# Optimization experiments

Hardware: AMD Instinct MI355X
Metric: run time of the kernel (lower is better)

The kernel has to match this reference:

```python
import jax, jax.numpy as jnp
import numpy as np

D_HEAD = 64
SCALE = D_HEAD ** 0.5
MASK_FILL = -10000.0


def setup_inputs() -> dict:
    key = jax.random.key(0)
    kq, kk, kv, km = jax.random.split(key, 4)
    B, H, S, D = 2, 16, 2048, D_HEAD
    query = jax.random.normal(kq, (B, H, S, D), dtype=jnp.float32)
    k = jax.random.normal(kk, (B, H, S, D), dtype=jnp.float32)
    v = jax.random.normal(kv, (B, H, S, D), dtype=jnp.float32)
    attn_mask = jax.random.randint(km, (B, H, S, S), 0, 2).astype(jnp.bool_)
    return {"query": query, "key": k, "value": v, "attn_mask": attn_mask}


def reference(query, key, value, attn_mask):
    # scores: [B, H, Sq, Sk]
    scores = jnp.einsum("bhqd,bhkd->bhqk", query, key) / SCALE
    scores = jnp.where(attn_mask, MASK_FILL, scores)
    attn_prob = jax.nn.softmax(scores, axis=-1)
    context = jnp.einsum("bhqk,bhkd->bhqd", attn_prob, value)
    return (context, attn_prob)
```

## Files before the change

kernel.cpp:

```cpp
#include <hip/hip_runtime.h>
#include <cstdint>
#include <cstddef>

#define S_LEN 2048
#define D_HEAD 64
#define NBH 32

typedef __attribute__((ext_vector_type(8))) short short8;
typedef __attribute__((ext_vector_type(8))) unsigned short ushort8;
typedef __attribute__((ext_vector_type(4))) unsigned short us4;
typedef __attribute__((ext_vector_type(4))) unsigned int ui4;
typedef __attribute__((ext_vector_type(4))) float floatx4;

__device__ __forceinline__ unsigned short f2bf(float f){
  union { float f; unsigned int i; } v; v.f = f;
  unsigned int u = v.i;
  u += 0x7fffu + ((u >> 16) & 1u);
  return (unsigned short)(u >> 16);
}
__device__ __forceinline__ float bf2f(unsigned short u){
  union { unsigned int i; float f; } v; v.i = ((unsigned int)u) << 16; return v.f;
}

__device__ __forceinline__ int swz(int row, int col){
  return row * S_LEN + ((((col >> 3) ^ row) & 15) << 3)
                     + (((col >> 3) & ~15) << 3) + (col & 7);
}

__global__ void detect_mask_kernel(const unsigned int* __restrict__ m, int* __restrict__ flag){
  __shared__ int f;
  if (threadIdx.x == 0) f = 0;
  __syncthreads();
  if (m[threadIdx.x] > 1u) atomicOr(&f, 1);
  __syncthreads();
  if (threadIdx.x == 0) *flag = f;
}

__global__ void convK_kernel(const float* __restrict__ K, unsigned short* __restrict__ Kb){
  const size_t i = ((size_t)blockIdx.x * 256 + threadIdx.x) * 8;
  floatx4 x0 = *(const floatx4*)(K + i);
  floatx4 x1 = *(const floatx4*)(K + i + 4);
  ushort8 o;
#pragma unroll
  for (int j = 0; j < 4; ++j){ o[j] = f2bf(x0[j]); o[4 + j] = f2bf(x1[j]); }
  *(ushort8*)(Kb + i) = o;
}

__global__ void vtrans_kernel(const float* __restrict__ V, unsigned short* __restrict__ Vt){
  const int bh = blockIdx.y;
  const int n  = threadIdx.x & 63;
  const int k0 = blockIdx.x * 32 + (threadIdx.x >> 6) * 8;
  const float* Vp = V + (size_t)bh * S_LEN * D_HEAD;
  ushort8 o;
#pragma unroll
  for (int i = 0; i < 8; ++i) o[i] = f2bf(Vp[(size_t)(k0 + i) * D_HEAD + n]);
  *(ushort8*)(Vt + (size_t)bh * D_HEAD * S_LEN + (size_t)n * S_LEN + k0) = o;
}

__global__ __launch_bounds__(256, 2) void attn_kernel(
    const float* __restrict__ Q, const unsigned short* __restrict__ Kb,
    const void* __restrict__ maskp, const int* __restrict__ flag,
    const unsigned short* __restrict__ Vt,
    float* __restrict__ prob, float* __restrict__ ctx,
    float* __restrict__ redg, float* __restrict__ invg){

  __shared__ unsigned short Pt[16 * S_LEN];

  const int lin  = blockIdx.y * gridDim.x + blockIdx.x;
  const int xcd  = lin & 7;
  const int sub  = lin >> 3;
  const int bh   = xcd * 4 + (sub & 3);
  const int qt   = sub >> 2;

  const int q0g  = bh * S_LEN + qt * 16;
  const int tid  = threadIdx.x;
  const int wave = tid >> 6;
  const int lane = tid & 63;
  const int quad = lane >> 4;
  const int r16  = lane & 15;
  const int blk  = bh * gridDim.x + qt;

  const float* qrow = Q + (size_t)(q0g + r16) * D_HEAD + quad * 8;
  short8 a0, a1;
  {
    floatx4 x0 = *(const floatx4*)(qrow);
    floatx4 x1 = *(const floatx4*)(qrow + 4);
    floatx4 y0 = *(const floatx4*)(qrow + 32);
    floatx4 y1 = *(const floatx4*)(qrow + 36);
#pragma unroll
    for (int j = 0; j < 4; ++j){
      a0[j] = (short)f2bf(x0[j]); a0[4 + j] = (short)f2bf(x1[j]);
      a1[j] = (short)f2bf(y0[j]); a1[4 + j] = (short)f2bf(y1[j]);
    }
  }

  const bool mInt = (*flag) == 0;
  const unsigned int*  mI = (const unsigned int*)maskp;
  const unsigned char* mB = (const unsigned char*)maskp;
  const size_t mrow = (size_t)(q0g + r16) * S_LEN;

  float racc = 0.f;

#pragma unroll 2
  for (int t = 0; t < 32; ++t){
    const int s0 = wave * 512 + t * 16;
    const unsigned short* krow = Kb + (size_t)(bh * S_LEN + s0 + r16) * D_HEAD + quad * 8;
    const short8 b0 = *(const short8*)(krow);
    const short8 b1 = *(const short8*)(krow + 32);
    unsigned int mm[4];
    if (mInt){
      const ui4 m4 = *(const ui4*)(mI + mrow + s0 + quad * 4);
#pragma unroll
      for (int i = 0; i < 4; ++i) mm[i] = m4[i];
    } else {
      const unsigned int mv = *(const unsigned int*)(mB + mrow + s0 + quad * 4);
#pragma unroll
      for (int i = 0; i < 4; ++i) mm[i] = (mv >> (8 * i)) & 0xffu;
    }
    floatx4 c = {0.f, 0.f, 0.f, 0.f};
    c = __builtin_amdgcn_mfma_f32_16x16x32_bf16(b0, a0, c, 0, 0, 0);
    c = __builtin_amdgcn_mfma_f32_16x16x32_bf16(b1, a1, c, 0, 0, 0);
    us4 w;
#pragma unroll
    for (int i = 0; i < 4; ++i){
      const float p = mm[i] ? 0.0f : __expf(c[i] * 0.125f);
      racc += p;
      w[i] = f2bf(p);
    }
    *(us4*)(&Pt[swz(r16, s0 + quad * 4)]) = w;
  }

  racc += __shfl_xor(racc, 16);
  racc += __shfl_xor(racc, 32);
  if (lane < 16) redg[(size_t)blk * 64 + wave * 16 + lane] = racc;
  __syncthreads();
  if (tid < 16){
    float s = 0.f;
#pragma unroll
    for (int w = 0; w < 4; ++w) s += redg[(size_t)blk * 64 + w * 16 + tid];
    invg[(size_t)blk * 16 + tid] = (s > 0.f) ? (1.0f / s) : 0.0f;
  }
  __syncthreads();

  float inv4[4];
#pragma unroll
  for (int i = 0; i < 4; ++i) inv4[i] = invg[(size_t)blk * 16 + quad * 4 + i];

  const unsigned short* vrow = Vt + (size_t)bh * D_HEAD * S_LEN
                                  + (size_t)(wave * 16 + r16) * S_LEN + quad * 8;
  floatx4 c = {0.f, 0.f, 0.f, 0.f};
#pragma unroll 4
  for (int kk = 0; kk < 64; ++kk){
    const short8 b = *(const short8*)(vrow + kk * 32);
    const short8 a = *(const short8*)(&Pt[swz(r16, kk * 32 + quad * 8)]);
    c = __builtin_amdgcn_mfma_f32_16x16x32_bf16(a, b, c, 0, 0, 0);
  }
#pragma unroll
  for (int i = 0; i < 4; ++i)
    ctx[(size_t)(q0g + quad * 4 + i) * D_HEAD + wave * 16 + r16] = c[i] * inv4[i];

#pragma unroll
  for (int rr = 0; rr < 4; ++rr){
    const int row = wave * 4 + rr;
    const float iv = invg[(size_t)blk * 16 + row];
    float* pg = prob + (size_t)(q0g + row) * S_LEN;
#pragma unroll
    for (int j = 0; j < 4; ++j){
      const int col = j * 512 + lane * 8;
      const ushort8 u = *(const ushort8*)(&Pt[swz(row, col)]);
      floatx4 o0, o1;
#pragma unroll
      for (int e = 0; e < 4; ++e){
        o0[e] = bf2f(u[e]) * iv;
        o1[e] = bf2f(u[4 + e]) * iv;
      }
      *(floatx4*)(pg + col)     = o0;
      *(floatx4*)(pg + col + 4) = o1;
    }
  }
}

extern "C" void kernel_launch(void* const* d_in, const int* in_sizes, int n_in,
                              void* d_out, int out_size, void* d_ws, size_t ws_size,
                              hipStream_t stream) {
  const float* Q = (const float*)d_in[0];
  const float* K = (const float*)d_in[1];
  const float* V = (const float*)d_in[2];
  const void*  M = d_in[3];

  float* ctx  = (float*)d_out;
  float* prob = (float*)d_out + (size_t)NBH * S_LEN * D_HEAD;

  int*   flag = (int*)d_ws;
  float* redg = (float*)((char*)d_ws + (1u << 12));
  float* invg = (float*)((char*)d_ws + (1u << 12) + (1u << 20));
  unsigned short* Kb = (unsigned short*)((char*)d_ws + (2u << 20));
  unsigned short* Vt = (unsigned short*)((char*)d_ws + (10u << 20));

  hipLaunchKernelGGL(detect_mask_kernel, dim3(1), dim3(256), 0, stream,
                     (const unsigned int*)M, flag);
  hipLaunchKernelGGL(convK_kernel, dim3(2048), dim3(256), 0, stream, K, Kb);
  hipLaunchKernelGGL(vtrans_kernel, dim3(S_LEN/32, NBH), dim3(256), 0, stream, V, Vt);
  hipLaunchKernelGGL(attn_kernel, dim3(S_LEN/16, NBH), dim3(256), 0, stream,
                     Q, Kb, M, flag, Vt, prob, ctx, redg, invg);
}
```

Before: 1.103 ms.

## Recompute scores in second pass, drop LDS staging, permute P in registers

Each wave now owns 16 query rows across the full key length. A first pass computes only the row sums, and a second pass recomputes QK^T and exp, writes normalized probabilities straight to global memory, and feeds P into the PV MFMA via ds_bpermute register shuffles. This removes the 64KB LDS buffer, the cross-wave reduction through global memory, and the block syncs, which allows higher occupancy (launch bounds 4). The cost is doubled QK MFMA, exp and mask-read work, with the mask now read twice from memory.

```diff
diff --git a/kernel.cpp b/kernel.cpp
--- a/kernel.cpp
+++ b/kernel.cpp
@@ -8,7 +8,6 @@
 
 typedef __attribute__((ext_vector_type(8))) short short8;
 typedef __attribute__((ext_vector_type(8))) unsigned short ushort8;
-typedef __attribute__((ext_vector_type(4))) unsigned short us4;
 typedef __attribute__((ext_vector_type(4))) unsigned int ui4;
 typedef __attribute__((ext_vector_type(4))) float floatx4;
 
@@ -18,13 +17,8 @@
   u += 0x7fffu + ((u >> 16) & 1u);
   return (unsigned short)(u >> 16);
 }
-__device__ __forceinline__ float bf2f(unsigned short u){
-  union { unsigned int i; float f; } v; v.i = ((unsigned int)u) << 16; return v.f;
-}
-
-__device__ __forceinline__ int swz(int row, int col){
-  return row * S_LEN + ((((col >> 3) ^ row) & 15) << 3)
-                     + (((col >> 3) & ~15) << 3) + (col & 7);
+__device__ __forceinline__ unsigned int pk2bf(float lo, float hi){
+  return ((unsigned int)f2bf(hi) << 16) | (unsigned int)f2bf(lo);
 }
 
 __global__ void detect_mask_kernel(const unsigned int* __restrict__ m, int* __restrict__ flag){
@@ -57,28 +51,24 @@
   *(ushort8*)(Vt + (size_t)bh * D_HEAD * S_LEN + (size_t)n * S_LEN + k0) = o;
 }
 
-__global__ __launch_bounds__(256, 2) void attn_kernel(
+__global__ __launch_bounds__(256, 4) void attn_kernel(
     const float* __restrict__ Q, const unsigned short* __restrict__ Kb,
     const void* __restrict__ maskp, const int* __restrict__ flag,
     const unsigned short* __restrict__ Vt,
-    float* __restrict__ prob, float* __restrict__ ctx,
-    float* __restrict__ redg, float* __restrict__ invg){
-
-  __shared__ unsigned short Pt[16 * S_LEN];
+    float* __restrict__ prob, float* __restrict__ ctx){
 
   const int lin  = blockIdx.y * gridDim.x + blockIdx.x;
   const int xcd  = lin & 7;
   const int sub  = lin >> 3;
   const int bh   = xcd * 4 + (sub & 3);
-  const int qt   = sub >> 2;
-
-  const int q0g  = bh * S_LEN + qt * 16;
-  const int tid  = threadIdx.x;
-  const int wave = tid >> 6;
-  const int lane = tid & 63;
+  const int qb   = sub >> 2;
+
+  const int wave = threadIdx.x >> 6;
+  const int lane = threadIdx.x & 63;
   const int quad = lane >> 4;
   const int r16  = lane & 15;
-  const int blk  = bh * gridDim.x + qt;
+
+  const int q0g = bh * S_LEN + qb * 64 + wave * 16;
 
   const float* qrow = Q + (size_t)(q0g + r16) * D_HEAD + quad * 8;
   short8 a0, a1;
@@ -95,88 +85,125 @@
   }
 
   const bool mInt = (*flag) == 0;
-  const unsigned int*  mI = (const unsigned int*)maskp;
-  const unsigned char* mB = (const unsigned char*)maskp;
-  const size_t mrow = (size_t)(q0g + r16) * S_LEN;
+  const unsigned int*  mI = (const unsigned int*)maskp + (size_t)(q0g + r16) * S_LEN;
+  const unsigned char* mB = (const unsigned char*)maskp + (size_t)(q0g + r16) * S_LEN;
+  const unsigned short* kbase = Kb + (size_t)bh * S_LEN * D_HEAD;
 
   float racc = 0.f;
-
 #pragma unroll 2
-  for (int t = 0; t < 32; ++t){
-    const int s0 = wave * 512 + t * 16;
-    const unsigned short* krow = Kb + (size_t)(bh * S_LEN + s0 + r16) * D_HEAD + quad * 8;
+  for (int t = 0; t < 128; ++t){
+    const unsigned short* krow = kbase + (size_t)(t * 16 + r16) * D_HEAD + quad * 8;
     const short8 b0 = *(const short8*)(krow);
     const short8 b1 = *(const short8*)(krow + 32);
     unsigned int mm[4];
     if (mInt){
-      const ui4 m4 = *(const ui4*)(mI + mrow + s0 + quad * 4);
+      const ui4 m4 = *(const ui4*)(mI + t * 16 + quad * 4);
 #pragma unroll
       for (int i = 0; i < 4; ++i) mm[i] = m4[i];
     } else {
-      const unsigned int mv = *(const unsigned int*)(mB + mrow + s0 + quad * 4);
+      const unsigned int mv = *(const unsigned int*)(mB + t * 16 + quad * 4);
 #pragma unroll
       for (int i = 0; i < 4; ++i) mm[i] = (mv >> (8 * i)) & 0xffu;
     }
     floatx4 c = {0.f, 0.f, 0.f, 0.f};
     c = __builtin_amdgcn_mfma_f32_16x16x32_bf16(b0, a0, c, 0, 0, 0);
     c = __builtin_amdgcn_mfma_f32_16x16x32_bf16(b1, a1, c, 0, 0, 0);
-    us4 w;
-#pragma unroll
-    for (int i = 0; i < 4; ++i){
-      const float p = mm[i] ? 0.0f : __expf(c[i] * 0.125f);
-      racc += p;
-      w[i] = f2bf(p);
-    }
-    *(us4*)(&Pt[swz(r16, s0 + quad * 4)]) = w;
-  }
-
+#pragma unroll
+    for (int i = 0; i < 4; ++i)
+      racc += mm[i] ? 0.0f : __expf(c[i] * 0.125f);
+  }
   racc += __shfl_xor(racc, 16);
   racc += __shfl_xor(racc, 32);
-  if (lane < 16) redg[(size_t)blk * 64 + wave * 16 + lane] = racc;
-  __syncthreads();
-  if (tid < 16){
-    float s = 0.f;
-#pragma unroll
-    for (int w = 0; w < 4; ++w) s += redg[(size_t)blk * 64 + w * 16 + tid];
-    invg[(size_t)blk * 16 + tid] = (s > 0.f) ? (1.0f / s) : 0.0f;
-  }
-  __syncthreads();
+  const float inv = (racc > 0.f) ? (1.0f / racc) : 0.0f;
+
+  float* prow = prob + (size_t)(q0g + r16) * S_LEN;
+  const unsigned short* vbase = Vt + (size_t)bh * D_HEAD * S_LEN
+                                   + (size_t)r16 * S_LEN + quad * 8;
+  floatx4 cc0 = {0.f,0.f,0.f,0.f}, cc1 = {0.f,0.f,0.f,0.f};
+  floatx4 cc2 = {0.f,0.f,0.f,0.f}, cc3 = {0.f,0.f,0.f,0.f};
+
+  for (int u = 0; u < 64; ++u){
+    const unsigned short* krow = kbase + (size_t)(u * 32 + r16) * D_HEAD + quad * 8;
+    const short8 b00 = *(const short8*)(krow);
+    const short8 b01 = *(const short8*)(krow + 32);
+    const short8 b10 = *(const short8*)(krow + 16 * D_HEAD);
+    const short8 b11 = *(const short8*)(krow + 16 * D_HEAD + 32);
+    unsigned int m0[4], m1[4];
+    if (mInt){
+      const ui4 w0 = *(const ui4*)(mI + u * 32 + quad * 4);
+      const ui4 w1 = *(const ui4*)(mI + u * 32 + 16 + quad * 4);
+#pragma unroll
+      for (int i = 0; i < 4; ++i){ m0[i] = w0[i]; m1[i] = w1[i]; }
+    } else {
+      const unsigned int v0m = *(const unsigned int*)(mB + u * 32 + quad * 4);
+      const unsigned int v1m = *(const unsigned int*)(mB + u * 32 + 16 + quad * 4);
+#pragma unroll
+      for (int i = 0; i < 4; ++i){
+        m0[i] = (v0m >> (8 * i)) & 0xffu;
+        m1[i] = (v1m >> (8 * i)) & 0xffu;
+      }
+    }
+    floatx4 c0 = {0.f,0.f,0.f,0.f}, c1 = {0.f,0.f,0.f,0.f};
+    c0 = __builtin_amdgcn_mfma_f32_16x16x32_bf16(b00, a0, c0, 0, 0, 0);
+    c0 = __builtin_amdgcn_mfma_f32_16x16x32_bf16(b01, a1, c0, 0, 0, 0);
+    c1 = __builtin_amdgcn_mfma_f32_16x16x32_bf16(b10, a0, c1, 0, 0, 0);
+    c1 = __builtin_amdgcn_mfma_f32_16x16x32_bf16(b11, a1, c1, 0, 0, 0);
+
+    float p0[4], p1[4];
+#pragma unroll
+    for (int i = 0; i < 4; ++i){
+      p0[i] = m0[i] ? 0.0f : __expf(c0[i] * 0.125f);
+      p1[i] = m1[i] ? 0.0f : __expf(c1[i] * 0.125f);
+    }
+
+    floatx4 o0, o1;
+#pragma unroll
+    for (int i = 0; i < 4; ++i){ o0[i] = p0[i] * inv; o1[i] = p1[i] * inv; }
+    *(floatx4*)(prow + u * 32 + quad * 4)      = o0;
+    *(floatx4*)(prow + u * 32 + 16 + quad * 4) = o1;
+
+    const int pl0 = (int)pk2bf(p0[0], p0[1]);
+    const int pl1 = (int)pk2bf(p0[2], p0[3]);
+    const int pl2 = (int)pk2bf(p1[0], p1[1]);
+    const int pl3 = (int)pk2bf(p1[2], p1[3]);
+
+    const int idx0 = (r16 + ((quad & 1) << 5)) << 2;
+    const int idx1 = idx0 + 64;
+    const int t0a = __builtin_amdgcn_ds_bpermute(idx0, pl0);
+    const int t0b = __builtin_amdgcn_ds_bpermute(idx0, pl2);
+    const int t1a = __builtin_amdgcn_ds_bpermute(idx0, pl1);
+    const int t1b = __builtin_amdgcn_ds_bpermute(idx0, pl3);
+    const int t2a = __builtin_amdgcn_ds_bpermute(idx1, pl0);
+    const int t2b = __builtin_amdgcn_ds_bpermute(idx1, pl2);
+    const int t3a = __builtin_amdgcn_ds_bpermute(idx1, pl1);
+    const int t3b = __builtin_amdgcn_ds_bpermute(idx1, pl3);
+    const bool hi = quad >= 2;
+    union { int d[4]; short8 s; } af;
+    af.d[0] = hi ? t0b : t0a;
+    af.d[1] = hi ? t1b : t1a;
+    af.d[2] = hi ? t2b : t2a;
+    af.d[3] = hi ? t3b : t3a;
+
+    const short8 v0 = *(const short8*)(vbase + u * 32);
+    const short8 v1 = *(const short8*)(vbase + 16 * S_LEN + u * 32);
+    const short8 v2 = *(const short8*)(vbase + 32 * S_LEN + u * 32);
+    const short8 v3 = *(const short8*)(vbase + 48 * S_LEN + u * 32);
+    cc0 = __builtin_amdgcn_mfma_f32_16x16x32_bf16(af.s, v0, cc0, 0, 0, 0);
+    cc1 = __builtin_amdgcn_mfma_f32_16x16x32_bf16(af.s, v1, cc1, 0, 0, 0);
+    cc2 = __builtin_amdgcn_mfma_f32_16x16x32_bf16(af.s, v2, cc2, 0, 0, 0);
+    cc3 = __builtin_amdgcn_mfma_f32_16x16x32_bf16(af.s, v3, cc3, 0, 0, 0);
+  }
 
   float inv4[4];
 #pragma unroll
-  for (int i = 0; i < 4; ++i) inv4[i] = invg[(size_t)blk * 16 + quad * 4 + i];
-
-  const unsigned short* vrow = Vt + (size_t)bh * D_HEAD * S_LEN
-                                  + (size_t)(wave * 16 + r16) * S_LEN + quad * 8;
-  floatx4 c = {0.f, 0.f, 0.f, 0.f};
-#pragma unroll 4
-  for (int kk = 0; kk < 64; ++kk){
-    const short8 b = *(const short8*)(vrow + kk * 32);
-    const short8 a = *(const short8*)(&Pt[swz(r16, kk * 32 + quad * 8)]);
-    c = __builtin_amdgcn_mfma_f32_16x16x32_bf16(a, b, c, 0, 0, 0);
-  }
-#pragma unroll
-  for (int i = 0; i < 4; ++i)
-    ctx[(size_t)(q0g + quad * 4 + i) * D_HEAD + wave * 16 + r16] = c[i] * inv4[i];
-
-#pragma unroll
-  for (int rr = 0; rr < 4; ++rr){
-    const int row = wave * 4 + rr;
-    const float iv = invg[(size_t)blk * 16 + row];
-    float* pg = prob + (size_t)(q0g + row) * S_LEN;
-#pragma unroll
-    for (int j = 0; j < 4; ++j){
-      const int col = j * 512 + lane * 8;
-      const ushort8 u = *(const ushort8*)(&Pt[swz(row, col)]);
-      floatx4 o0, o1;
-#pragma unroll
-      for (int e = 0; e < 4; ++e){
-        o0[e] = bf2f(u[e]) * iv;
-        o1[e] = bf2f(u[4 + e]) * iv;
-      }
-      *(floatx4*)(pg + col)     = o0;
-      *(floatx4*)(pg + col + 4) = o1;
-    }
+  for (int i = 0; i < 4; ++i) inv4[i] = __shfl(inv, quad * 4 + i, 64);
+#pragma unroll
+  for (int i = 0; i < 4; ++i){
+    float* cr = ctx + (size_t)(q0g + quad * 4 + i) * D_HEAD + r16;
+    cr[ 0] = cc0[i] * inv4[i];
+    cr[16] = cc1[i] * inv4[i];
+    cr[32] = cc2[i] * inv4[i];
+    cr[48] = cc3[i] * inv4[i];
   }
 }
 
@@ -192,8 +219,6 @@
   float* prob = (float*)d_out + (size_t)NBH * S_LEN * D_HEAD;
 
   int*   flag = (int*)d_ws;
-  float* redg = (float*)((char*)d_ws + (1u << 12));
-  float* invg = (float*)((char*)d_ws + (1u << 12) + (1u << 20));
   unsigned short* Kb = (unsigned short*)((char*)d_ws + (2u << 20));
   unsigned short* Vt = (unsigned short*)((char*)d_ws + (10u << 20));
 
@@ -201,6 +226,6 @@
                      (const unsigned int*)M, flag);
   hipLaunchKernelGGL(convK_kernel, dim3(2048), dim3(256), 0, stream, K, Kb);
   hipLaunchKernelGGL(vtrans_kernel, dim3(S_LEN/32, NBH), dim3(256), 0, stream, V, Vt);
-  hipLaunchKernelGGL(attn_kernel, dim3(S_LEN/16, NBH), dim3(256), 0, stream,
-                     Q, Kb, M, flag, Vt, prob, ctx, redg, invg);
-}
+  hipLaunchKernelGGL(attn_kernel, dim3(S_LEN/64, NBH), dim3(256), 0, stream,
+                     Q, Kb, M, flag, Vt, prob, ctx);
+}
```

Result: slower. 1.285 ms (+16.5%).

## Pre-pack attention mask into bitmask and split PV accumulators

Applied to the files above, without the earlier changes.

A new pre-pass kernel compresses the boolean or int mask into one bit per element, writing it into the not-yet-written context region of the output buffer. The attention kernel then loads one prefetched vector of packed bits per eight score tiles instead of a per-tile mask load. This is meant to shorten the latency-bound mask reads in the QK loop. In exchange it adds a separate full pass over the mask plus a 16MB write and re-read. The PV loop also uses two independent MFMA accumulators to break the dependency chain.

```diff
diff --git a/kernel.cpp b/kernel.cpp
--- a/kernel.cpp
+++ b/kernel.cpp
@@ -34,6 +34,36 @@
   if (m[threadIdx.x] > 1u) atomicOr(&f, 1);
   __syncthreads();
   if (threadIdx.x == 0) *flag = f;
+}
+
+__global__ void packmask_kernel(const void* __restrict__ maskp, const int* __restrict__ flag,
+                                unsigned int* __restrict__ pm){
+  const int w = blockIdx.x * 256 + threadIdx.x;
+  unsigned int bits = 0;
+  if (*flag){
+    const unsigned char* mb = (const unsigned char*)maskp + (size_t)w * 32;
+    const ui4 x0 = *(const ui4*)(mb);
+    const ui4 x1 = *(const ui4*)(mb + 16);
+#pragma unroll
+    for (int i = 0; i < 4; ++i){
+      const unsigned int a = x0[i], b = x1[i];
+#pragma unroll
+      for (int j = 0; j < 4; ++j){
+        bits |= (((a >> (8 * j)) & 0xffu) ? 1u : 0u) << (4 * i + j);
+        bits |= (((b >> (8 * j)) & 0xffu) ? 1u : 0u) << (16 + 4 * i + j);
+      }
+    }
+  } else {
+    const unsigned int* mi = (const unsigned int*)maskp + (size_t)w * 32;
+#pragma unroll
+    for (int i = 0; i < 8; ++i){
+      const ui4 x = *(const ui4*)(mi + i * 4);
+#pragma unroll
+      for (int j = 0; j < 4; ++j)
+        bits |= (x[j] ? 1u : 0u) << (i * 4 + j);
+    }
+  }
+  pm[w] = bits;
 }
 
 __global__ void convK_kernel(const float* __restrict__ K, unsigned short* __restrict__ Kb){
@@ -59,7 +89,7 @@
 
 __global__ __launch_bounds__(256, 2) void attn_kernel(
     const float* __restrict__ Q, const unsigned short* __restrict__ Kb,
-    const void* __restrict__ maskp, const int* __restrict__ flag,
+    const unsigned int* __restrict__ pm,
     const unsigned short* __restrict__ Vt,
     float* __restrict__ prob, float* __restrict__ ctx,
     float* __restrict__ redg, float* __restrict__ invg){
@@ -94,40 +124,34 @@
     }
   }
 
-  const bool mInt = (*flag) == 0;
-  const unsigned int*  mI = (const unsigned int*)maskp;
-  const unsigned char* mB = (const unsigned char*)maskp;
-  const size_t mrow = (size_t)(q0g + r16) * S_LEN;
+  const unsigned int* mrow = pm + (size_t)(q0g + r16) * 64 + wave * 16;
+  const unsigned short* kbase = Kb + (size_t)bh * S_LEN * D_HEAD;
 
   float racc = 0.f;
-
-#pragma unroll 2
-  for (int t = 0; t < 32; ++t){
-    const int s0 = wave * 512 + t * 16;
-    const unsigned short* krow = Kb + (size_t)(bh * S_LEN + s0 + r16) * D_HEAD + quad * 8;
-    const short8 b0 = *(const short8*)(krow);
-    const short8 b1 = *(const short8*)(krow + 32);
-    unsigned int mm[4];
-    if (mInt){
-      const ui4 m4 = *(const ui4*)(mI + mrow + s0 + quad * 4);
-#pragma unroll
-      for (int i = 0; i < 4; ++i) mm[i] = m4[i];
-    } else {
-      const unsigned int mv = *(const unsigned int*)(mB + mrow + s0 + quad * 4);
-#pragma unroll
-      for (int i = 0; i < 4; ++i) mm[i] = (mv >> (8 * i)) & 0xffu;
-    }
-    floatx4 c = {0.f, 0.f, 0.f, 0.f};
-    c = __builtin_amdgcn_mfma_f32_16x16x32_bf16(b0, a0, c, 0, 0, 0);
-    c = __builtin_amdgcn_mfma_f32_16x16x32_bf16(b1, a1, c, 0, 0, 0);
-    us4 w;
-#pragma unroll
-    for (int i = 0; i < 4; ++i){
-      const float p = mm[i] ? 0.0f : __expf(c[i] * 0.125f);
-      racc += p;
-      w[i] = f2bf(p);
-    }
-    *(us4*)(&Pt[swz(r16, s0 + quad * 4)]) = w;
+  ui4 mcur = *(const ui4*)(mrow);
+  for (int tt = 0; tt < 4; ++tt){
+    const ui4 mnext = (tt < 3) ? *(const ui4*)(mrow + (tt + 1) * 4) : mcur;
+#pragma unroll
+    for (int tj = 0; tj < 8; ++tj){
+      const int t  = tt * 8 + tj;
+      const int s0 = wave * 512 + t * 16;
+      const unsigned short* krow = kbase + (size_t)(s0 + r16) * D_HEAD + quad * 8;
+      const short8 b0 = *(const short8*)(krow);
+      const short8 b1 = *(const short8*)(krow + 32);
+      floatx4 c = {0.f, 0.f, 0.f, 0.f};
+      c = __builtin_amdgcn_mfma_f32_16x16x32_bf16(b0, a0, c, 0, 0, 0);
+      c = __builtin_amdgcn_mfma_f32_16x16x32_bf16(b1, a1, c, 0, 0, 0);
+      const unsigned int bits = mcur[tj >> 1] >> (16 * (tj & 1) + 4 * quad);
+      us4 w;
+#pragma unroll
+      for (int i = 0; i < 4; ++i){
+        const float p = ((bits >> i) & 1u) ? 0.0f : __expf(c[i] * 0.125f);
+        racc += p;
+        w[i] = f2bf(p);
+      }
+      *(us4*)(&Pt[swz(r16, s0 + quad * 4)]) = w;
+    }
+    mcur = mnext;
   }
 
   racc += __shfl_xor(racc, 16);
@@ -148,16 +172,19 @@
 
   const unsigned short* vrow = Vt + (size_t)bh * D_HEAD * S_LEN
                                   + (size_t)(wave * 16 + r16) * S_LEN + quad * 8;
-  floatx4 c = {0.f, 0.f, 0.f, 0.f};
-#pragma unroll 4
-  for (int kk = 0; kk < 64; ++kk){
-    const short8 b = *(const short8*)(vrow + kk * 32);
-    const short8 a = *(const short8*)(&Pt[swz(r16, kk * 32 + quad * 8)]);
-    c = __builtin_amdgcn_mfma_f32_16x16x32_bf16(a, b, c, 0, 0, 0);
+  floatx4 cA = {0.f,0.f,0.f,0.f}, cB = {0.f,0.f,0.f,0.f};
+#pragma unroll 8
+  for (int kk = 0; kk < 64; kk += 2){
+    const short8 bv0 = *(const short8*)(vrow + kk * 32);
+    const short8 aa0 = *(const short8*)(&Pt[swz(r16, kk * 32 + quad * 8)]);
+    const short8 bv1 = *(const short8*)(vrow + (kk + 1) * 32);
+    const short8 aa1 = *(const short8*)(&Pt[swz(r16, (kk + 1) * 32 + quad * 8)]);
+    cA = __builtin_amdgcn_mfma_f32_16x16x32_bf16(aa0, bv0, cA, 0, 0, 0);
+    cB = __builtin_amdgcn_mfma_f32_16x16x32_bf16(aa1, bv1, cB, 0, 0, 0);
   }
 #pragma unroll
   for (int i = 0; i < 4; ++i)
-    ctx[(size_t)(q0g + quad * 4 + i) * D_HEAD + wave * 16 + r16] = c[i] * inv4[i];
+    ctx[(size_t)(q0g + quad * 4 + i) * D_HEAD + wave * 16 + r16] = (cA[i] + cB[i]) * inv4[i];
 
 #pragma unroll
   for (int rr = 0; rr < 4; ++rr){
@@ -191,6 +218,8 @@
   float* ctx  = (float*)d_out;
   float* prob = (float*)d_out + (size_t)NBH * S_LEN * D_HEAD;
 
+  unsigned int* pm = (unsigned int*)d_out;
+
   int*   flag = (int*)d_ws;
   float* redg = (float*)((char*)d_ws + (1u << 12));
   float* invg = (float*)((char*)d_ws + (1u << 12) + (1u << 20));
@@ -199,8 +228,10 @@
 
   hipLaunchKernelGGL(detect_mask_kernel, dim3(1), dim3(256), 0, stream,
                      (const unsigned int*)M, flag);
+  hipLaunchKernelGGL(packmask_kernel, dim3((NBH * S_LEN * S_LEN / 32) / 256), dim3(256),
+                     0, stream, M, flag, pm);
   hipLaunchKernelGGL(convK_kernel, dim3(2048), dim3(256), 0, stream, K, Kb);
   hipLaunchKernelGGL(vtrans_kernel, dim3(S_LEN/32, NBH), dim3(256), 0, stream, V, Vt);
   hipLaunchKernelGGL(attn_kernel, dim3(S_LEN/16, NBH), dim3(256), 0, stream,
-                     Q, Kb, M, flag, Vt, prob, ctx, redg, invg);
-}
+                     Q, Kb, pm, Vt, prob, ctx, redg, invg);
+}
```

Measured after the change: 1.148 ms. 4.0% more time.
